# Kernel tuning notes

Measured on AMD Instinct MI355X. Metric: run time of the kernel, lower is better.

## Reference

```python
import jax, jax.numpy as jnp
import numpy as np

B, L, DIN, DT, NOUT = 2, 144, 1024, 150, 4


def setup_inputs() -> dict:
    key = jax.random.key(0)
    ks = jax.random.split(key, 7)
    w = lambda k, shape: (jax.random.normal(k, shape, jnp.float32) * 0.02)
    return dict(
        x=jax.random.normal(ks[0], (B, L, DIN), jnp.float32),
        W_sh=w(ks[1], (DIN, DT)), b_sh=jnp.zeros((DT,), jnp.float32),
        W_st=w(ks[2], (DIN, DT)), b_st=jnp.zeros((DT,), jnp.float32),
        W_oh=w(ks[3], (DIN, DT)), b_oh=jnp.zeros((DT,), jnp.float32),
        W_ot=w(ks[4], (DIN, DT)), b_ot=jnp.zeros((DT,), jnp.float32),
        W_tri1=w(ks[5], (NOUT, DT, DT, DT)),
        W_tri2=w(ks[6], (NOUT, DT, DT, DT)),
    )


def _triaffine(x, y, z, W):
    # supar Triaffine convention: out[b,z,x,y,o] = sum_{i,k,j} x[b,x,i] W[o,i,k,j] y[b,y,j] z[b,z,k]
    w = jnp.einsum('bzk,oikj->bzoij', z, W)      # [B,L,o,d,d]
    t = jnp.einsum('bzoij,byj->bzoiy', w, y)     # [B,L,o,d,L]
    return jnp.einsum('bzoiy,bxi->bzxyo', t, x)  # [B,L,L,L,o]


def reference(x, W_sh, b_sh, W_st, b_st, W_oh, b_oh, W_ot, b_ot, W_tri1, W_tri2):
    # MLP projections (dropout is identity at eval time)
    sh = x @ W_sh + b_sh
    st = x @ W_st + b_st
    oh = x @ W_oh + b_oh
    ot = x @ W_ot + b_ot
    n = x.shape[1]
    # torch .triu() on (..., sh, st) keeps entries with sh <= st, zeros the rest
    tri = jnp.arange(n)[:, None] <= jnp.arange(n)[None, :]
    m = tri[None, :, :, None, None]
    # shstoh = Triaffine(st, rel_oh, sh) -> [b, sh, st, oh, o]; triu over (sh, st)
    s1 = _triaffine(st, oh, sh, W_tri1)
    s1 = jnp.where(m, s1, 0.0)
    # shstot = Triaffine(rel_ot, st, sh) -> [b, sh, ot, st, o]; permutes give (b, sh, st, ot, o) with triu over (sh, st)
    s2 = _triaffine(ot, st, sh, W_tri2)
    s2 = jnp.where(m, jnp.transpose(s2, (0, 1, 3, 2, 4)), 0.0)
    return jax.nn.log_softmax(s1, axis=-1), jax.nn.log_softmax(s2, axis=-1)
```

## Files before the change

kernel.cpp:

```cpp
#include <hip/hip_runtime.h>
#include <hip/hip_bf16.h>
#include <math.h>

typedef unsigned short u16;
typedef __attribute__((ext_vector_type(8))) short bf16x8;
typedef __attribute__((ext_vector_type(8))) unsigned short us8;
typedef __attribute__((ext_vector_type(4))) float f32x4;

static __device__ __forceinline__ u16 f2bf(float f) {
  __hip_bfloat16 h = __float2bfloat16(f);
  return *reinterpret_cast<u16*>(&h);
}

__global__ __launch_bounds__(256) void conv_x(const float* __restrict__ x,
                                              u16* __restrict__ xb) {
  int idx = (blockIdx.x * 256 + threadIdx.x) * 4;
  float4 v = *(const float4*)(x + idx);
  ushort4 o;
  o.x = f2bf(v.x); o.y = f2bf(v.y); o.z = f2bf(v.z); o.w = f2bf(v.w);
  *(ushort4*)(xb + idx) = o;
}

__global__ __launch_bounds__(256) void trans_wp(
    const float* __restrict__ W0, const float* __restrict__ W1,
    const float* __restrict__ W2, const float* __restrict__ W3,
    u16* __restrict__ WT4) {
  __shared__ float lds[64 * 151];
  int kt = blockIdx.x, p = blockIdx.y;
  const float* W = (p == 0) ? W0 : (p == 1) ? W1 : (p == 2) ? W2 : W3;
  for (int t = threadIdx.x; t < 64 * 150; t += 256) {
    int k = t / 150, j = t - k * 150;
    lds[k * 151 + j] = W[(size_t)(kt * 64 + k) * 150 + j];
  }
  __syncthreads();
  u16* dst = WT4 + (size_t)p * 160 * 1024 + kt * 64;
  for (int t = threadIdx.x; t < 160 * 64; t += 256) {
    int j = t >> 6, kk = t & 63;
    float v = (j < 150) ? lds[kk * 151 + j] : 0.f;
    dst[(size_t)j * 1024 + kk] = f2bf(v);
  }
}

__global__ __launch_bounds__(256) void transw2(const float* __restrict__ Wa,
                                               const float* __restrict__ Wb,
                                               u16* __restrict__ WtT) {
  __shared__ float lds[150 * 82];
  int oi = blockIdx.x, jh = blockIdx.y, tri = blockIdx.z;
  const float* W = tri ? Wb : Wa;
  const float* src = W + (size_t)oi * 22500 + jh * 80;
  for (int t = threadIdx.x; t < 150 * 40; t += 256) {
    int k = t / 40, c = t - k * 40;
    if (jh * 80 + 2 * c < 150) {
      float2 v = *(const float2*)(src + (size_t)k * 150 + 2 * c);
      *(float2*)&lds[k * 82 + 2 * c] = v;
    }
  }
  __syncthreads();
  u16* dst = WtT + (size_t)tri * 15360000 + (size_t)oi * 25600 +
             (size_t)jh * 80 * 160;
  for (int t = threadIdx.x; t < 80 * 20; t += 256) {
    int jl = t / 20, kc = t - jl * 20;
    int j = jh * 80 + jl;
    bool jlive = (j < 150);
    us8 v;
#pragma unroll
    for (int u = 0; u < 8; ++u) {
      int k = kc * 8 + u;
      float f = (jlive && k < 150) ? lds[k * 82 + jl] : 0.f;
      v[u] = f2bf(f);
    }
    *(us8*)(dst + (size_t)jl * 160 + kc * 8) = v;
  }
}

template <int STAGE>
__global__ __launch_bounds__(192) void gemm_sw(
    const u16* __restrict__ M0, const u16* __restrict__ N0,
    u16* __restrict__ C, const float* __restrict__ bias0,
    const float* __restrict__ bias1, const float* __restrict__ bias2,
    const float* __restrict__ bias3) {
  constexpr int KS = (STAGE == 0) ? 32 : 5;
  constexpr int SR = (STAGE == 0) ? 1024 : 160;
  const u16* Mb;
  const u16* Nb;
  u16* Cb = nullptr;
  if (STAGE == 0) {
    Mb = M0 + (size_t)blockIdx.x * 80 * 1024;
    Nb = N0 + (size_t)blockIdx.y * 144 * 1024;
  } else if (STAGE == 1) {
    int nt = blockIdx.x, oip = blockIdx.y, b = blockIdx.z;
    int tri = (oip >= 600) ? 1 : 0;
    int oi = oip - tri * 600;
    int o = oi / 150, i = oi - o * 150;
    Mb = M0 + (size_t)oip * 25600 + nt * 12800;
    Nb = N0 + (size_t)b * 23040;
    Cb = C + (size_t)tri * 29491200 + (size_t)b * 14745600 +
         ((size_t)o * 160 + i) * 160 + nt * 80;
  } else {
    int nt = blockIdx.x, f2p = blockIdx.y, b = blockIdx.z;
    int tri = (f2p >= 576) ? 1 : 0;
    int f2 = f2p - tri * 576;
    int z = f2 >> 2, o = f2 & 3;
    Mb = M0 + (size_t)tri * 29491200 + (size_t)b * 14745600 +
         (size_t)z * 102400 + o * 25600 + nt * 12800;
    Nb = N0 + (size_t)(tri ? 46080 : 92160) + (size_t)b * 23040;
    Cb = C + (size_t)tri * 26542080 + (size_t)b * 13271040 +
         (size_t)z * 92160 + o * 23040 + nt * 80;
  }
  int tid = threadIdx.x;
  int lane = tid & 63, wave = tid >> 6;
  int l16 = lane & 15, quad = lane >> 4;
  const u16* Mp = Mb + (size_t)l16 * SR + quad * 8;
  const u16* Np = Nb + (size_t)(wave * 48 + l16) * SR + quad * 8;
  f32x4 acc[5][3];
#pragma unroll
  for (int mi = 0; mi < 5; ++mi)
#pragma unroll
    for (int ni = 0; ni < 3; ++ni) acc[mi][ni] = (f32x4){0.f, 0.f, 0.f, 0.f};

#pragma unroll
  for (int ks = 0; ks < KS; ++ks) {
    bf16x8 mf[5], nf[3];
#pragma unroll
    for (int mi = 0; mi < 5; ++mi)
      mf[mi] = *(const bf16x8*)(Mp + (size_t)mi * 16 * SR + ks * 32);
#pragma unroll
    for (int ni = 0; ni < 3; ++ni)
      nf[ni] = *(const bf16x8*)(Np + (size_t)ni * 16 * SR + ks * 32);
#pragma unroll
    for (int mi = 0; mi < 5; ++mi)
#pragma unroll
      for (int ni = 0; ni < 3; ++ni)
        acc[mi][ni] = __builtin_amdgcn_mfma_f32_16x16x32_bf16(
            mf[mi], nf[ni], acc[mi][ni], 0, 0, 0);
  }

  if (STAGE == 0) {
    int p = blockIdx.x >> 1;
    const float* bp =
        (p == 0) ? bias0 : (p == 1) ? bias1 : (p == 2) ? bias2 : bias3;
    int jb0 = (blockIdx.x & 1) * 80;
#pragma unroll
    for (int mi = 0; mi < 5; ++mi) {
      int jb = jb0 + mi * 16 + quad * 4;
#pragma unroll
      for (int ni = 0; ni < 3; ++ni) {
        int row = blockIdx.y * 144 + wave * 48 + ni * 16 + l16;
        ushort4 pk;
        float v0 = (jb + 0 < 150) ? acc[mi][ni][0] + bp[jb + 0] : 0.f;
        float v1 = (jb + 1 < 150) ? acc[mi][ni][1] + bp[jb + 1] : 0.f;
        float v2 = (jb + 2 < 150) ? acc[mi][ni][2] + bp[jb + 2] : 0.f;
        float v3 = (jb + 3 < 150) ? acc[mi][ni][3] + bp[jb + 3] : 0.f;
        pk.x = f2bf(v0); pk.y = f2bf(v1); pk.z = f2bf(v2); pk.w = f2bf(v3);
        *(ushort4*)(C + ((size_t)p * 288 + row) * 160 + jb) = pk;
      }
    }
  } else {
#pragma unroll
    for (int mi = 0; mi < 5; ++mi) {
      int mb4 = mi * 16 + quad * 4;
#pragma unroll
      for (int ni = 0; ni < 3; ++ni) {
        int outer = wave * 48 + ni * 16 + l16;
        ushort4 pk;
        pk.x = f2bf(acc[mi][ni][0]); pk.y = f2bf(acc[mi][ni][1]);
        pk.z = f2bf(acc[mi][ni][2]); pk.w = f2bf(acc[mi][ni][3]);
        size_t off = (STAGE == 1) ? ((size_t)outer * 102400 + mb4)
                                  : ((size_t)outer * 160 + mb4);
        *(ushort4*)(Cb + off) = pk;
      }
    }
  }
}

template <int VAR>
__global__ __launch_bounds__(256) void stage3_kernel(
    const u16* __restrict__ tb, const u16* __restrict__ P,
    float* __restrict__ out, int BT) {
  __shared__ float sf[9216];
  int bx = blockIdx.x;
  int b = bx & 1, xt = (bx >> 1) * 48;
  int yt = blockIdx.y * 48;
  int zg = blockIdx.z;
  int tid = threadIdx.x;
  const float NL4 = -1.3862943611198906f;
  size_t obase = ((size_t)(b * 144 + zg)) * 82944;
  if (zg > xt + 47) {
    float4 v = make_float4(NL4, NL4, NL4, NL4);
    for (int p = tid; p < 2304; p += 256) {
      int xl = p / 48, yl = p - xl * 48;
      *(float4*)(out + obase + ((size_t)(xt + xl) * 144 + yt + yl) * 4) = v;
    }
    return;
  }
  int pbase = (VAR == 0) ? xt : yt;
  int qbase = (VAR == 0) ? yt : xt;
  int lane = tid & 63, o = tid >> 6, l16 = lane & 15, quad = lane >> 4;
  const u16* Pp = P + (size_t)b * 23040 + (size_t)(pbase + l16) * 160 + quad * 8;
  const u16* Tp = tb + (size_t)b * BT + (size_t)zg * 92160 +
                  (size_t)(o * 144 + qbase + l16) * 160 + quad * 8;
  const u16* Ap = (VAR == 0) ? Pp : Tp;
  const u16* Bp = (VAR == 0) ? Tp : Pp;
  f32x4 acc[3][3];
#pragma unroll
  for (int mi = 0; mi < 3; ++mi)
#pragma unroll
    for (int ni = 0; ni < 3; ++ni) acc[mi][ni] = (f32x4){0.f, 0.f, 0.f, 0.f};

#pragma unroll
  for (int ks = 0; ks < 5; ++ks) {
    bf16x8 af[3], bfr[3];
#pragma unroll
    for (int mi = 0; mi < 3; ++mi)
      af[mi] = *(const bf16x8*)(Ap + (size_t)mi * 16 * 160 + ks * 32);
#pragma unroll
    for (int ni = 0; ni < 3; ++ni)
      bfr[ni] = *(const bf16x8*)(Bp + (size_t)ni * 16 * 160 + ks * 32);
#pragma unroll
    for (int mi = 0; mi < 3; ++mi)
#pragma unroll
      for (int ni = 0; ni < 3; ++ni)
        acc[mi][ni] = __builtin_amdgcn_mfma_f32_16x16x32_bf16(
            af[mi], bfr[ni], acc[mi][ni], 0, 0, 0);
  }

#pragma unroll
  for (int mi = 0; mi < 3; ++mi)
#pragma unroll
    for (int ni = 0; ni < 3; ++ni)
#pragma unroll
      for (int r = 0; r < 4; ++r)
        sf[((mi * 16 + quad * 4 + r) * 48 + ni * 16 + l16) * 4 + o] =
            acc[mi][ni][r];
  __syncthreads();
  for (int p = tid; p < 2304; p += 256) {
    int xl = p / 48, yl = p - xl * 48;
    int xg = xt + xl;
    float4 v;
    if (zg > xg) {
      v = make_float4(NL4, NL4, NL4, NL4);
    } else {
      float c0 = sf[p * 4], c1 = sf[p * 4 + 1];
      float c2 = sf[p * 4 + 2], c3 = sf[p * 4 + 3];
      float mx = fmaxf(fmaxf(c0, c1), fmaxf(c2, c3));
      float l = mx + logf(expf(c0 - mx) + expf(c1 - mx) + expf(c2 - mx) +
                          expf(c3 - mx));
      v = make_float4(c0 - l, c1 - l, c2 - l, c3 - l);
    }
    *(float4*)(out + obase + ((size_t)xg * 144 + yt + yl) * 4) = v;
  }
}

extern "C" void kernel_launch(void* const* d_in, const int* in_sizes, int n_in,
                              void* d_out, int out_size, void* d_ws,
                              size_t ws_size, hipStream_t stream) {
  const float* x = (const float*)d_in[0];
  const float* Wsh = (const float*)d_in[1];
  const float* bsh = (const float*)d_in[2];
  const float* Wst = (const float*)d_in[3];
  const float* bst = (const float*)d_in[4];
  const float* Woh = (const float*)d_in[5];
  const float* boh = (const float*)d_in[6];
  const float* Wot = (const float*)d_in[7];
  const float* bot = (const float*)d_in[8];
  const float* Wt1 = (const float*)d_in[9];
  const float* Wt2 = (const float*)d_in[10];

  u16* ws = (u16*)d_ws;
  u16* xb = ws;
  u16* WT4 = ws + 294912;
  u16* pAll = ws + 950272;
  u16* WtT = ws + 1134592;
  u16* wbuf = ws + 31854592;
  u16* tbuf = ws + 90836992;
  (void)ws_size;

  conv_x<<<288, 256, 0, stream>>>(x, xb);
  trans_wp<<<dim3(16, 4), 256, 0, stream>>>(Wsh, Wst, Woh, Wot, WT4);
  transw2<<<dim3(600, 2, 2), 256, 0, stream>>>(Wt1, Wt2, WtT);
  gemm_sw<0><<<dim3(8, 2), 192, 0, stream>>>(WT4, xb, pAll, bsh, bst, boh,
                                             bot);
  gemm_sw<1><<<dim3(2, 1200, 2), 192, 0, stream>>>(WtT, pAll, wbuf, nullptr,
                                                   nullptr, nullptr, nullptr);
  gemm_sw<2><<<dim3(2, 1152, 2), 192, 0, stream>>>(wbuf, pAll, tbuf, nullptr,
                                                   nullptr, nullptr, nullptr);

  float* out0 = (float*)d_out;
  float* out1 = out0 + 23887872;
  stage3_kernel<0><<<dim3(6, 3, 144), 256, 0, stream>>>(
      tbuf, pAll + 46080, out0, 13271040);
  stage3_kernel<1><<<dim3(6, 3, 144), 256, 0, stream>>>(
      tbuf + 26542080, pAll + 138240, out1, 13271040);
}
```

Baseline: 621.5 us.

## Map the output index into MFMA A rows so log-softmax runs from registers

Stage 3 loads its A operand with rows interleaved across the four output classes: each 16-row MFMA tile now covers 4 spatial rows times 4 outputs. Each lane's accumulator vector therefore holds all four class scores for one (x,y) point. The epilogue does log-softmax directly on those registers and stores one float4 per point. This removes the 36 KB shared-memory staging buffer and the block barrier, which should raise occupancy, at the cost of more scattered global A loads and output stores.

```diff
diff --git a/kernel.cpp b/kernel.cpp
--- a/kernel.cpp
+++ b/kernel.cpp
@@ -177,7 +177,6 @@
 __global__ __launch_bounds__(256) void stage3_kernel(
     const u16* __restrict__ tb, const u16* __restrict__ P,
     float* __restrict__ out, int BT) {
-  __shared__ float sf[9216];
   int bx = blockIdx.x;
   int b = bx & 1, xt = (bx >> 1) * 48;
   int yt = blockIdx.y * 48;
@@ -193,14 +192,15 @@
     }
     return;
   }
-  int pbase = (VAR == 0) ? xt : yt;
-  int qbase = (VAR == 0) ? yt : xt;
-  int lane = tid & 63, o = tid >> 6, l16 = lane & 15, quad = lane >> 4;
-  const u16* Pp = P + (size_t)b * 23040 + (size_t)(pbase + l16) * 160 + quad * 8;
-  const u16* Tp = tb + (size_t)b * BT + (size_t)zg * 92160 +
-                  (size_t)(o * 144 + qbase + l16) * 160 + quad * 8;
-  const u16* Ap = (VAR == 0) ? Pp : Tp;
-  const u16* Bp = (VAR == 0) ? Tp : Pp;
+  int lane = tid & 63, wave = tid >> 6, l16 = lane & 15, quad = lane >> 4;
+  int o = l16 & 3, rq = l16 >> 2;
+  int arow0 = (VAR == 0) ? yt : xt;
+  int nrow0 = (VAR == 0) ? xt : yt;
+  const u16* Ap = tb + (size_t)b * BT + (size_t)zg * 92160 +
+                  (size_t)o * 23040 +
+                  (size_t)(arow0 + wave * 12 + rq) * 160 + quad * 8;
+  const u16* Bp =
+      P + (size_t)b * 23040 + (size_t)(nrow0 + l16) * 160 + quad * 8;
   f32x4 acc[3][3];
 #pragma unroll
   for (int mi = 0; mi < 3; ++mi)
@@ -212,7 +212,7 @@
     bf16x8 af[3], bfr[3];
 #pragma unroll
     for (int mi = 0; mi < 3; ++mi)
-      af[mi] = *(const bf16x8*)(Ap + (size_t)mi * 16 * 160 + ks * 32);
+      af[mi] = *(const bf16x8*)(Ap + (size_t)mi * 4 * 160 + ks * 32);
 #pragma unroll
     for (int ni = 0; ni < 3; ++ni)
       bfr[ni] = *(const bf16x8*)(Bp + (size_t)ni * 16 * 160 + ks * 32);
@@ -225,29 +225,26 @@
   }
 
 #pragma unroll
-  for (int mi = 0; mi < 3; ++mi)
-#pragma unroll
-    for (int ni = 0; ni < 3; ++ni)
-#pragma unroll
-      for (int r = 0; r < 4; ++r)
-        sf[((mi * 16 + quad * 4 + r) * 48 + ni * 16 + l16) * 4 + o] =
-            acc[mi][ni][r];
-  __syncthreads();
-  for (int p = tid; p < 2304; p += 256) {
-    int xl = p / 48, yl = p - xl * 48;
-    int xg = xt + xl;
-    float4 v;
-    if (zg > xg) {
-      v = make_float4(NL4, NL4, NL4, NL4);
-    } else {
-      float c0 = sf[p * 4], c1 = sf[p * 4 + 1];
-      float c2 = sf[p * 4 + 2], c3 = sf[p * 4 + 3];
-      float mx = fmaxf(fmaxf(c0, c1), fmaxf(c2, c3));
-      float l = mx + logf(expf(c0 - mx) + expf(c1 - mx) + expf(c2 - mx) +
-                          expf(c3 - mx));
-      v = make_float4(c0 - l, c1 - l, c2 - l, c3 - l);
-    }
-    *(float4*)(out + obase + ((size_t)xg * 144 + yt + yl) * 4) = v;
+  for (int mi = 0; mi < 3; ++mi) {
+    int arow = arow0 + wave * 12 + mi * 4 + quad;
+#pragma unroll
+    for (int ni = 0; ni < 3; ++ni) {
+      int nrow = nrow0 + ni * 16 + l16;
+      int xg = (VAR == 0) ? nrow : arow;
+      int yg = (VAR == 0) ? arow : nrow;
+      float4 v;
+      if (zg > xg) {
+        v = make_float4(NL4, NL4, NL4, NL4);
+      } else {
+        float c0 = acc[mi][ni][0], c1 = acc[mi][ni][1];
+        float c2 = acc[mi][ni][2], c3 = acc[mi][ni][3];
+        float mx = fmaxf(fmaxf(c0, c1), fmaxf(c2, c3));
+        float l = mx + logf(expf(c0 - mx) + expf(c1 - mx) + expf(c2 - mx) +
+                            expf(c3 - mx));
+        v = make_float4(c0 - l, c1 - l, c2 - l, c3 - l);
+      }
+      *(float4*)(out + obase + ((size_t)xg * 144 + yg) * 4) = v;
+    }
   }
 }
 
```

Result: no change. 631.5 us (+1.6%).
